# Kernel tuning notes

Measured on AMD Instinct MI355X. Metric: run time of the kernel, lower is better.

## Reference

```python
import jax, jax.numpy as jnp
import numpy as np

NUM_EMBEDDINGS = 1024
EMBEDDING_DIM = 64
COMMITMENT_COST = 0.25


def setup_inputs() -> dict:
    key = jax.random.key(0)
    k1, k2 = jax.random.split(key)
    z = jax.random.normal(k1, (32, 32, 32, EMBEDDING_DIM), dtype=jnp.float32)
    # embedding.weight.data.uniform_(-1/num_embeddings, 1/num_embeddings)
    lim = 1.0 / NUM_EMBEDDINGS
    codebook = jax.random.uniform(k2, (NUM_EMBEDDINGS, EMBEDDING_DIM),
                                  dtype=jnp.float32, minval=-lim, maxval=lim)
    return {"z": z, "codebook": codebook}


def reference(z, codebook):
    beta = COMMITMENT_COST
    zf = z.reshape(-1, EMBEDDING_DIM)                      # [N, D]
    # Squared euclidean distances (argmin is invariant to sqrt in torch.cdist)
    d2 = (jnp.sum(zf * zf, axis=1, keepdims=True)          # [N, 1]
          + jnp.sum(codebook * codebook, axis=1)[None, :]  # [1, K]
          - 2.0 * jnp.einsum('nd,kd->nk', zf, codebook))   # [N, K]
    encoding_indices = jnp.argmin(d2, axis=1)              # [N] int32
    z_q = codebook[encoding_indices].reshape(z.shape)      # [..., D]
    sg = jax.lax.stop_gradient
    loss = jnp.mean((sg(z_q) - z) ** 2) + beta * jnp.mean((z_q - sg(z)) ** 2)
    z_q_st = z + sg(z_q - z)                               # straight-through
    return (z_q_st, loss, encoding_indices)
```

## Files before the change

kernel.cpp:

```cpp
#include <hip/hip_runtime.h>
#include <stdint.h>

#define N_ROWS 32768
#define DIM 64
#define K_CODES 1024
#define ROWS_PER_BLOCK 128
#define THREADS 512
#define CHUNK 256
#define NCHUNK (K_CODES / CHUNK)
#define NBLOCKS (N_ROWS / ROWS_PER_BLOCK)
#define N_ELEMS (N_ROWS * DIM)
#define ZT_STRIDE 128
#define CT_STRIDE 256


__device__ __forceinline__ float bfbits(uint32_t b) { return __uint_as_float(b << 16); }
__device__ __forceinline__ float bf_lo(uint32_t u) { return __uint_as_float(u << 16); }
__device__ __forceinline__ float bf_hi(uint32_t u) { return __uint_as_float(u & 0xFFFF0000u); }

__device__ __forceinline__ float round_bf16(float f) {
  uint32_t u = __float_as_uint(f);
  uint32_t r = ((u + 0x7FFFu + ((u >> 16) & 1u)) >> 16) << 16;
  return __uint_as_float(r);
}

__device__ __forceinline__ int zcol(int row) {
  return ((row >> 3) << 2) + (((row >> 2) & 1) << 6) + (row & 3);
}

template <typename F>
__device__ __forceinline__ float np_sum64(F get) {
  float r0 = get(0), r1 = get(1), r2 = get(2), r3 = get(3);
  float r4 = get(4), r5 = get(5), r6 = get(6), r7 = get(7);
  for (int i = 8; i < 64; i += 8) {
    r0 = __fadd_rn(r0, get(i + 0)); r1 = __fadd_rn(r1, get(i + 1));
    r2 = __fadd_rn(r2, get(i + 2)); r3 = __fadd_rn(r3, get(i + 3));
    r4 = __fadd_rn(r4, get(i + 4)); r5 = __fadd_rn(r5, get(i + 5));
    r6 = __fadd_rn(r6, get(i + 6)); r7 = __fadd_rn(r7, get(i + 7));
  }
  return __fadd_rn(__fadd_rn(__fadd_rn(r0, r1), __fadd_rn(r2, r3)),
                   __fadd_rn(__fadd_rn(r4, r5), __fadd_rn(r6, r7)));
}

__global__ __launch_bounds__(THREADS, 1) void vq_kernel(
    const void* __restrict__ z, const void* __restrict__ cb,
    float* __restrict__ out, double* __restrict__ partials,
    unsigned int* __restrict__ counter) {
  const int tid = threadIdx.x;

  __shared__ int s_cnt[2];
  __shared__ int s_last;
  __shared__ float zt[DIM][ZT_STRIDE];
  __shared__ uint32_t ctu[DIM][CT_STRIDE];
  __shared__ float s_cc[K_CODES];
  __shared__ float s_zz[ROWS_PER_BLOCK];
  __shared__ float s_bestW[8][ROWS_PER_BLOCK];
  __shared__ int   s_kW[8][ROWS_PER_BLOCK];
  __shared__ int   s_win[ROWS_PER_BLOCK];
  __shared__ double s_loss[ROWS_PER_BLOCK];
  float (*ctf)[CT_STRIDE] = (float (*)[CT_STRIDE])ctu;

  if (tid < 2) s_cnt[tid] = 0;
  __syncthreads();
  if (tid < 128) {
    uint32_t wc = ((const uint32_t*)cb)[(size_t)tid * 255];
    float vc = fabsf(bfbits(wc & 0xFFFFu));
    if (vc == 0.0f || (vc > 5.9e-8f && vc < 32.0f)) atomicAdd(&s_cnt[1], 1);
    uint32_t wz = ((const uint32_t*)z)[(size_t)tid * 8191];
    float vz = fabsf(bfbits(wz & 0xFFFFu));
    if (vz == 0.0f || (vz > 5.9e-8f && vz < 32.0f)) atomicAdd(&s_cnt[0], 1);
  }
  __syncthreads();
  const bool z_bf16  = s_cnt[0] >= 96;
  const bool cb_bf16 = s_cnt[1] >= 96;

  const int TR = tid & 15;
  const int TK = tid >> 4;
  const size_t row0 = (size_t)blockIdx.x * ROWS_PER_BLOCK;

  for (int kk = tid; kk < K_CODES; kk += THREADS) {
    float r0, r1, r2, r3, r4, r5, r6, r7;
    if (cb_bf16) {
      const uint4* cp = (const uint4*)((const uint16_t*)cb + (size_t)kk * DIM);
      uint4 u = cp[0];
      r0 = __fmul_rn(bf_lo(u.x), bf_lo(u.x)); r1 = __fmul_rn(bf_hi(u.x), bf_hi(u.x));
      r2 = __fmul_rn(bf_lo(u.y), bf_lo(u.y)); r3 = __fmul_rn(bf_hi(u.y), bf_hi(u.y));
      r4 = __fmul_rn(bf_lo(u.z), bf_lo(u.z)); r5 = __fmul_rn(bf_hi(u.z), bf_hi(u.z));
      r6 = __fmul_rn(bf_lo(u.w), bf_lo(u.w)); r7 = __fmul_rn(bf_hi(u.w), bf_hi(u.w));
      #pragma unroll
      for (int j = 1; j < 8; ++j) {
        u = cp[j];
        r0 = __fadd_rn(r0, __fmul_rn(bf_lo(u.x), bf_lo(u.x)));
        r1 = __fadd_rn(r1, __fmul_rn(bf_hi(u.x), bf_hi(u.x)));
        r2 = __fadd_rn(r2, __fmul_rn(bf_lo(u.y), bf_lo(u.y)));
        r3 = __fadd_rn(r3, __fmul_rn(bf_hi(u.y), bf_hi(u.y)));
        r4 = __fadd_rn(r4, __fmul_rn(bf_lo(u.z), bf_lo(u.z)));
        r5 = __fadd_rn(r5, __fmul_rn(bf_hi(u.z), bf_hi(u.z)));
        r6 = __fadd_rn(r6, __fmul_rn(bf_lo(u.w), bf_lo(u.w)));
        r7 = __fadd_rn(r7, __fmul_rn(bf_hi(u.w), bf_hi(u.w)));
      }
    } else {
      const float4* cp = (const float4*)((const float*)cb + (size_t)kk * DIM);
      float4 a = cp[0], b = cp[1];
      r0 = __fmul_rn(a.x, a.x); r1 = __fmul_rn(a.y, a.y);
      r2 = __fmul_rn(a.z, a.z); r3 = __fmul_rn(a.w, a.w);
      r4 = __fmul_rn(b.x, b.x); r5 = __fmul_rn(b.y, b.y);
      r6 = __fmul_rn(b.z, b.z); r7 = __fmul_rn(b.w, b.w);
      #pragma unroll
      for (int j = 1; j < 8; ++j) {
        a = cp[2 * j]; b = cp[2 * j + 1];
        r0 = __fadd_rn(r0, __fmul_rn(a.x, a.x));
        r1 = __fadd_rn(r1, __fmul_rn(a.y, a.y));
        r2 = __fadd_rn(r2, __fmul_rn(a.z, a.z));
        r3 = __fadd_rn(r3, __fmul_rn(a.w, a.w));
        r4 = __fadd_rn(r4, __fmul_rn(b.x, b.x));
        r5 = __fadd_rn(r5, __fmul_rn(b.y, b.y));
        r6 = __fadd_rn(r6, __fmul_rn(b.z, b.z));
        r7 = __fadd_rn(r7, __fmul_rn(b.w, b.w));
      }
    }
    s_cc[kk] = __fadd_rn(__fadd_rn(__fadd_rn(r0, r1), __fadd_rn(r2, r3)),
                         __fadd_rn(__fadd_rn(r4, r5), __fadd_rn(r6, r7)));
  }

  if (z_bf16) {
    const uint4* src = (const uint4*)((const uint16_t*)z + row0 * DIM);
    #pragma unroll
    for (int j = 0; j < 2; ++j) {
      int idx = tid + THREADS * j;
      int row = idx >> 3, w = idx & 7, d0 = w * 8;
      int col = zcol(row) ^ (w << 2);
      uint4 u = src[idx];
      zt[d0 + 0][col] = bf_lo(u.x); zt[d0 + 1][col] = bf_hi(u.x);
      zt[d0 + 2][col] = bf_lo(u.y); zt[d0 + 3][col] = bf_hi(u.y);
      zt[d0 + 4][col] = bf_lo(u.z); zt[d0 + 5][col] = bf_hi(u.z);
      zt[d0 + 6][col] = bf_lo(u.w); zt[d0 + 7][col] = bf_hi(u.w);
    }
  } else {
    const float4* src = (const float4*)((const float*)z + row0 * DIM);
    #pragma unroll
    for (int j = 0; j < 4; ++j) {
      int idx = tid + THREADS * j;
      int row = idx >> 4, d0 = (idx & 15) * 4;
      int col = zcol(row) ^ (((d0 >> 3) & 7) << 2);
      float4 v = src[idx];
      zt[d0 + 0][col] = v.x; zt[d0 + 1][col] = v.y;
      zt[d0 + 2][col] = v.z; zt[d0 + 3][col] = v.w;
    }
  }
  __syncthreads();

  if (tid < ROWS_PER_BLOCK) {
    const int c0 = zcol(tid);
    s_zz[tid] = np_sum64([&](int d) {
      float v = zt[d][c0 ^ (((d >> 3) & 7) << 2)];
      return __fmul_rn(v, v); });
  }

  float best[8] = {3.4e38f, 3.4e38f, 3.4e38f, 3.4e38f,
                   3.4e38f, 3.4e38f, 3.4e38f, 3.4e38f};
  int bk[8] = {0, 0, 0, 0, 0, 0, 0, 0};
  float acc[8][8];
  #pragma unroll
  for (int ri = 0; ri < 8; ++ri)
    #pragma unroll
    for (int ki = 0; ki < 8; ++ki) acc[ri][ki] = 0.0f;

  if (cb_bf16) {
    for (int c = 0; c < NCHUNK; ++c) {
      __syncthreads();
      const uint4* src = (const uint4*)((const uint16_t*)cb + (size_t)c * CHUNK * DIM);
      #pragma unroll
      for (int t = 0; t < 2; ++t) {
        int task = tid + THREADS * t;
        int j = task >> 3, w = task & 7;
        uint4 a = src[(size_t)(2 * j) * 8 + w];
        uint4 b = src[(size_t)(2 * j + 1) * 8 + w];
        int d0 = w * 8;
        int colb = j ^ (w << 3);
        ctu[d0 + 0][colb] = (a.x & 0xFFFFu) | (b.x << 16);
        ctu[d0 + 1][colb] = (a.x >> 16) | (b.x & 0xFFFF0000u);
        ctu[d0 + 2][colb] = (a.y & 0xFFFFu) | (b.y << 16);
        ctu[d0 + 3][colb] = (a.y >> 16) | (b.y & 0xFFFF0000u);
        ctu[d0 + 4][colb] = (a.z & 0xFFFFu) | (b.z << 16);
        ctu[d0 + 5][colb] = (a.z >> 16) | (b.z & 0xFFFF0000u);
        ctu[d0 + 6][colb] = (a.w & 0xFFFFu) | (b.w << 16);
        ctu[d0 + 7][colb] = (a.w >> 16) | (b.w & 0xFFFF0000u);
      }
      __syncthreads();

      #pragma unroll 4
      for (int d = 0; d < DIM; ++d) {
        const int zs = ((d >> 3) & 7) << 2;
        const int X  = (d >> 3) << 3;
        float4 zA = *(const float4*)&zt[d][(TR << 2) ^ zs];
        float4 zB = *(const float4*)&zt[d][((TR << 2) ^ zs) + 64];
        uint4 cu = *(const uint4*)&ctu[d][(TK << 2) ^ X];
        float zv[8] = {zA.x, zA.y, zA.z, zA.w, zB.x, zB.y, zB.z, zB.w};
        float cv[8] = {bf_lo(cu.x), bf_hi(cu.x), bf_lo(cu.y), bf_hi(cu.y),
                       bf_lo(cu.z), bf_hi(cu.z), bf_lo(cu.w), bf_hi(cu.w)};
        #pragma unroll
        for (int ri = 0; ri < 8; ++ri)
          #pragma unroll
          for (int ki = 0; ki < 8; ++ki)
            acc[ri][ki] = __fadd_rn(acc[ri][ki], __fmul_rn(zv[ri], cv[ki]));
      }

      #pragma unroll
      for (int ri = 0; ri < 8; ++ri) {
        const float zzr = s_zz[TR * 8 + ri];
        #pragma unroll
        for (int ki = 0; ki < 8; ++ki) {
          const int k = c * CHUNK + TK * 8 + ki;
          float e = __fsub_rn(__fadd_rn(zzr, s_cc[k]), __fmul_rn(2.0f, acc[ri][ki]));
          if (e < best[ri]) { best[ri] = e; bk[ri] = k; }
          acc[ri][ki] = 0.0f;
        }
      }
    }
  } else {
    for (int c = 0; c < NCHUNK; ++c) {
      __syncthreads();
      const float4* src = (const float4*)((const float*)cb + (size_t)c * CHUNK * DIM);
      #pragma unroll
      for (int j = 0; j < 8; ++j) {
        int idx = tid + THREADS * j;
        int kc = idx >> 4, d0 = (idx & 15) * 4;
        int col = kc ^ (((d0 >> 3) & 3) << 3);
        float4 v = src[idx];
        ctf[d0 + 0][col] = v.x; ctf[d0 + 1][col] = v.y;
        ctf[d0 + 2][col] = v.z; ctf[d0 + 3][col] = v.w;
      }
      __syncthreads();

      #pragma unroll 4
      for (int d = 0; d < DIM; ++d) {
        const int zs = ((d >> 3) & 7) << 2;
        const int cs = ((d >> 3) & 3) << 3;
        float4 zA = *(const float4*)&zt[d][(TR << 2) ^ zs];
        float4 zB = *(const float4*)&zt[d][((TR << 2) ^ zs) + 64];
        float4 cA = *(const float4*)&ctf[d][(TK << 3) ^ cs];
        float4 cB = *(const float4*)&ctf[d][((TK << 3) ^ cs) + 4];
        float zv[8] = {zA.x, zA.y, zA.z, zA.w, zB.x, zB.y, zB.z, zB.w};
        float cv[8] = {cA.x, cA.y, cA.z, cA.w, cB.x, cB.y, cB.z, cB.w};
        #pragma unroll
        for (int ri = 0; ri < 8; ++ri)
          #pragma unroll
          for (int ki = 0; ki < 8; ++ki)
            acc[ri][ki] = __fadd_rn(acc[ri][ki], __fmul_rn(zv[ri], cv[ki]));
      }

      #pragma unroll
      for (int ri = 0; ri < 8; ++ri) {
        const float zzr = s_zz[TR * 8 + ri];
        #pragma unroll
        for (int ki = 0; ki < 8; ++ki) {
          const int k = c * CHUNK + TK * 8 + ki;
          float e = __fsub_rn(__fadd_rn(zzr, s_cc[k]), __fmul_rn(2.0f, acc[ri][ki]));
          if (e < best[ri]) { best[ri] = e; bk[ri] = k; }
          acc[ri][ki] = 0.0f;
        }
      }
    }
  }

  #pragma unroll
  for (int ri = 0; ri < 8; ++ri) {
    float v = best[ri]; int k = bk[ri];
    {
      float v2 = __shfl_xor(v, 16, 64); int k2 = __shfl_xor(k, 16, 64);
      if (v2 < v || (v2 == v && k2 < k)) { v = v2; k = k2; }
      v2 = __shfl_xor(v, 32, 64); k2 = __shfl_xor(k, 32, 64);
      if (v2 < v || (v2 == v && k2 < k)) { v = v2; k = k2; }
    }
    best[ri] = v; bk[ri] = k;
  }
  {
    const int lane = tid & 63, wv = tid >> 6;
    if (lane < 16) {
      #pragma unroll
      for (int ri = 0; ri < 8; ++ri) {
        s_bestW[wv][lane * 8 + ri] = best[ri];
        s_kW[wv][lane * 8 + ri] = bk[ri];
      }
    }
  }
  __syncthreads();

  if (tid < ROWS_PER_BLOCK) {
    float b = 3.4e38f;
    int bbk = 0x7FFFFFFF;
    #pragma unroll
    for (int p = 0; p < 8; ++p) {
      float v = s_bestW[p][tid];
      int vk = s_kW[p][tid];
      if (v < b || (v == b && vk < bbk)) { b = v; bbk = vk; }
    }
    s_win[tid] = bbk;
    const int c0 = zcol(tid);
    double acc2 = 0.0;
    if (cb_bf16) {
      const uint16_t* cp = (const uint16_t*)cb + (size_t)bbk * DIM;
      for (int d = 0; d < DIM; ++d) {
        double df = (double)zt[d][c0 ^ (((d >> 3) & 7) << 2)]
                  - (double)bfbits((uint32_t)cp[d]);
        acc2 = fma(df, df, acc2);
      }
    } else {
      const float* cp = (const float*)cb + (size_t)bbk * DIM;
      for (int d = 0; d < DIM; ++d) {
        double df = (double)zt[d][c0 ^ (((d >> 3) & 7) << 2)] - (double)cp[d];
        acc2 = fma(df, df, acc2);
      }
    }
    s_loss[tid] = acc2;
    out[(size_t)N_ELEMS + 1 + row0 + tid] = round_bf16((float)bbk);
  }
  __syncthreads();

  const size_t base = row0 * DIM;
  #pragma unroll
  for (int j = 0; j < 16; ++j) {
    int idx = tid + THREADS * j;
    int rr = idx >> 6, dd = idx & 63;
    int w = s_win[rr];
    float v;
    if (cb_bf16) v = bfbits((uint32_t)((const uint16_t*)cb)[(size_t)w * DIM + dd]);
    else         v = round_bf16(((const float*)cb)[(size_t)w * DIM + dd]);
    out[base + idx] = v;
  }

  if (tid == 0) {
    double s = 0.0;
    for (int i = 0; i < ROWS_PER_BLOCK; ++i) s += s_loss[i];
    partials[blockIdx.x] = s;
    __threadfence();
    unsigned int old = atomicAdd(counter, 1u);
    s_last = (((old + 1u) % (unsigned int)NBLOCKS) == 0u) ? 1 : 0;
  }
  __syncthreads();
  if (s_last) {
    __threadfence();
    if (tid < 128) s_loss[tid] = partials[tid] + partials[tid + 128];
    __syncthreads();
    if (tid == 0) {
      double t = 0.0;
      for (int i = 0; i < 128; ++i) t += s_loss[i];
      out[N_ELEMS] = round_bf16((float)(1.25 * t / (double)N_ELEMS));
    }
  }
}

extern "C" void kernel_launch(void* const* d_in, const int* in_sizes, int n_in,
                              void* d_out, int out_size, void* d_ws, size_t ws_size,
                              hipStream_t stream) {
  const void* z  = d_in[0];
  const void* cb = d_in[1];
  float* out = (float*)d_out;
  uint8_t* ws = (uint8_t*)d_ws;
  unsigned int* counter = (unsigned int*)(ws + 4096);
  double* partials = (double*)(ws + 8192);

  vq_kernel<<<NBLOCKS, THREADS, 0, stream>>>(z, cb, out, partials, counter);
}
```

Measured before the change: 133.1 us.

## Halve rows per block to 64 and shrink per-thread register tile

Halves rows per block from 128 to 64, doubling the grid to 512 blocks so more CUs are busy, and shrinks each thread's accumulator tile from 8x8 to 4x8 (bf16) or 4x4 (fp32). The shared-memory swizzles are reworked for the narrower layouts, and the fp32 codebook path now streams 128-code chunks. The final partial-sum reduction is generalised to the larger block count. The cost is less register-level reuse per LDS load and more codebook staging traffic in total, since each block still reads the whole codebook for fewer rows.

```diff
diff --git a/kernel.cpp b/kernel.cpp
--- a/kernel.cpp
+++ b/kernel.cpp
@@ -4,14 +4,14 @@
 #define N_ROWS 32768
 #define DIM 64
 #define K_CODES 1024
-#define ROWS_PER_BLOCK 128
+#define ROWS_PER_BLOCK 64
 #define THREADS 512
 #define CHUNK 256
 #define NCHUNK (K_CODES / CHUNK)
 #define NBLOCKS (N_ROWS / ROWS_PER_BLOCK)
 #define N_ELEMS (N_ROWS * DIM)
-#define ZT_STRIDE 128
-#define CT_STRIDE 256
+#define ZT_STRIDE 64
+#define CT_STRIDE 128
 
 
 __device__ __forceinline__ float bfbits(uint32_t b) { return __uint_as_float(b << 16); }
@@ -22,10 +22,6 @@
   uint32_t u = __float_as_uint(f);
   uint32_t r = ((u + 0x7FFFu + ((u >> 16) & 1u)) >> 16) << 16;
   return __uint_as_float(r);
-}
-
-__device__ __forceinline__ int zcol(int row) {
-  return ((row >> 3) << 2) + (((row >> 2) & 1) << 6) + (row & 3);
 }
 
 template <typename F>
@@ -125,11 +121,10 @@
 
   if (z_bf16) {
     const uint4* src = (const uint4*)((const uint16_t*)z + row0 * DIM);
-    #pragma unroll
-    for (int j = 0; j < 2; ++j) {
-      int idx = tid + THREADS * j;
+    {
+      int idx = tid;
       int row = idx >> 3, w = idx & 7, d0 = w * 8;
-      int col = zcol(row) ^ (w << 2);
+      int col = row ^ (w << 3);
       uint4 u = src[idx];
       zt[d0 + 0][col] = bf_lo(u.x); zt[d0 + 1][col] = bf_hi(u.x);
       zt[d0 + 2][col] = bf_lo(u.y); zt[d0 + 3][col] = bf_hi(u.y);
@@ -139,10 +134,10 @@
   } else {
     const float4* src = (const float4*)((const float*)z + row0 * DIM);
     #pragma unroll
-    for (int j = 0; j < 4; ++j) {
+    for (int j = 0; j < 2; ++j) {
       int idx = tid + THREADS * j;
       int row = idx >> 4, d0 = (idx & 15) * 4;
-      int col = zcol(row) ^ (((d0 >> 3) & 7) << 2);
+      int col = row ^ (((d0 >> 3) & 7) << 3);
       float4 v = src[idx];
       zt[d0 + 0][col] = v.x; zt[d0 + 1][col] = v.y;
       zt[d0 + 2][col] = v.z; zt[d0 + 3][col] = v.w;
@@ -151,18 +146,16 @@
   __syncthreads();
 
   if (tid < ROWS_PER_BLOCK) {
-    const int c0 = zcol(tid);
     s_zz[tid] = np_sum64([&](int d) {
-      float v = zt[d][c0 ^ (((d >> 3) & 7) << 2)];
+      float v = zt[d][tid ^ (((d >> 3) & 7) << 3)];
       return __fmul_rn(v, v); });
   }
 
-  float best[8] = {3.4e38f, 3.4e38f, 3.4e38f, 3.4e38f,
-                   3.4e38f, 3.4e38f, 3.4e38f, 3.4e38f};
-  int bk[8] = {0, 0, 0, 0, 0, 0, 0, 0};
-  float acc[8][8];
+  float best[4] = {3.4e38f, 3.4e38f, 3.4e38f, 3.4e38f};
+  int bk[4] = {0, 0, 0, 0};
+  float acc[4][8];
   #pragma unroll
-  for (int ri = 0; ri < 8; ++ri)
+  for (int ri = 0; ri < 4; ++ri)
     #pragma unroll
     for (int ki = 0; ki < 8; ++ki) acc[ri][ki] = 0.0f;
 
@@ -191,24 +184,22 @@
 
       #pragma unroll 4
       for (int d = 0; d < DIM; ++d) {
-        const int zs = ((d >> 3) & 7) << 2;
-        const int X  = (d >> 3) << 3;
-        float4 zA = *(const float4*)&zt[d][(TR << 2) ^ zs];
-        float4 zB = *(const float4*)&zt[d][((TR << 2) ^ zs) + 64];
+        const int X = (d >> 3) << 3;
+        float4 zA = *(const float4*)&zt[d][(TR << 2) ^ X];
         uint4 cu = *(const uint4*)&ctu[d][(TK << 2) ^ X];
-        float zv[8] = {zA.x, zA.y, zA.z, zA.w, zB.x, zB.y, zB.z, zB.w};
+        float zv[4] = {zA.x, zA.y, zA.z, zA.w};
         float cv[8] = {bf_lo(cu.x), bf_hi(cu.x), bf_lo(cu.y), bf_hi(cu.y),
                        bf_lo(cu.z), bf_hi(cu.z), bf_lo(cu.w), bf_hi(cu.w)};
         #pragma unroll
-        for (int ri = 0; ri < 8; ++ri)
+        for (int ri = 0; ri < 4; ++ri)
           #pragma unroll
           for (int ki = 0; ki < 8; ++ki)
             acc[ri][ki] = __fadd_rn(acc[ri][ki], __fmul_rn(zv[ri], cv[ki]));
       }
 
       #pragma unroll
-      for (int ri = 0; ri < 8; ++ri) {
-        const float zzr = s_zz[TR * 8 + ri];
+      for (int ri = 0; ri < 4; ++ri) {
+        const float zzr = s_zz[TR * 4 + ri];
         #pragma unroll
         for (int ki = 0; ki < 8; ++ki) {
           const int k = c * CHUNK + TK * 8 + ki;
@@ -219,14 +210,14 @@
       }
     }
   } else {
-    for (int c = 0; c < NCHUNK; ++c) {
+    for (int hc = 0; hc < 8; ++hc) {
       __syncthreads();
-      const float4* src = (const float4*)((const float*)cb + (size_t)c * CHUNK * DIM);
-      #pragma unroll
-      for (int j = 0; j < 8; ++j) {
-        int idx = tid + THREADS * j;
+      const float4* src = (const float4*)((const float*)cb + (size_t)hc * 128 * DIM);
+      #pragma unroll
+      for (int t = 0; t < 4; ++t) {
+        int idx = tid + THREADS * t;
         int kc = idx >> 4, d0 = (idx & 15) * 4;
-        int col = kc ^ (((d0 >> 3) & 3) << 3);
+        int col = kc ^ (((d0 >> 3) & 7) << 2);
         float4 v = src[idx];
         ctf[d0 + 0][col] = v.x; ctf[d0 + 1][col] = v.y;
         ctf[d0 + 2][col] = v.z; ctf[d0 + 3][col] = v.w;
@@ -235,27 +226,25 @@
 
       #pragma unroll 4
       for (int d = 0; d < DIM; ++d) {
-        const int zs = ((d >> 3) & 7) << 2;
-        const int cs = ((d >> 3) & 3) << 3;
-        float4 zA = *(const float4*)&zt[d][(TR << 2) ^ zs];
-        float4 zB = *(const float4*)&zt[d][((TR << 2) ^ zs) + 64];
-        float4 cA = *(const float4*)&ctf[d][(TK << 3) ^ cs];
-        float4 cB = *(const float4*)&ctf[d][((TK << 3) ^ cs) + 4];
-        float zv[8] = {zA.x, zA.y, zA.z, zA.w, zB.x, zB.y, zB.z, zB.w};
-        float cv[8] = {cA.x, cA.y, cA.z, cA.w, cB.x, cB.y, cB.z, cB.w};
+        const int X3 = (d >> 3) << 3;
+        const int X2 = (d >> 3) << 2;
+        float4 zA = *(const float4*)&zt[d][(TR << 2) ^ X3];
+        float4 cA = *(const float4*)&ctf[d][(TK << 2) ^ X2];
+        float zv[4] = {zA.x, zA.y, zA.z, zA.w};
+        float cv[4] = {cA.x, cA.y, cA.z, cA.w};
         #pragma unroll
-        for (int ri = 0; ri < 8; ++ri)
+        for (int ri = 0; ri < 4; ++ri)
           #pragma unroll
-          for (int ki = 0; ki < 8; ++ki)
+          for (int ki = 0; ki < 4; ++ki)
             acc[ri][ki] = __fadd_rn(acc[ri][ki], __fmul_rn(zv[ri], cv[ki]));
       }
 
       #pragma unroll
-      for (int ri = 0; ri < 8; ++ri) {
-        const float zzr = s_zz[TR * 8 + ri];
+      for (int ri = 0; ri < 4; ++ri) {
+        const float zzr = s_zz[TR * 4 + ri];
         #pragma unroll
-        for (int ki = 0; ki < 8; ++ki) {
-          const int k = c * CHUNK + TK * 8 + ki;
+        for (int ki = 0; ki < 4; ++ki) {
+          const int k = hc * 128 + TK * 4 + ki;
           float e = __fsub_rn(__fadd_rn(zzr, s_cc[k]), __fmul_rn(2.0f, acc[ri][ki]));
           if (e < best[ri]) { best[ri] = e; bk[ri] = k; }
           acc[ri][ki] = 0.0f;
@@ -265,7 +254,7 @@
   }
 
   #pragma unroll
-  for (int ri = 0; ri < 8; ++ri) {
+  for (int ri = 0; ri < 4; ++ri) {
     float v = best[ri]; int k = bk[ri];
     {
       float v2 = __shfl_xor(v, 16, 64); int k2 = __shfl_xor(k, 16, 64);
@@ -279,9 +268,9 @@
     const int lane = tid & 63, wv = tid >> 6;
     if (lane < 16) {
       #pragma unroll
-      for (int ri = 0; ri < 8; ++ri) {
-        s_bestW[wv][lane * 8 + ri] = best[ri];
-        s_kW[wv][lane * 8 + ri] = bk[ri];
+      for (int ri = 0; ri < 4; ++ri) {
+        s_bestW[wv][lane * 4 + ri] = best[ri];
+        s_kW[wv][lane * 4 + ri] = bk[ri];
       }
     }
   }
@@ -297,19 +286,18 @@
       if (v < b || (v == b && vk < bbk)) { b = v; bbk = vk; }
     }
     s_win[tid] = bbk;
-    const int c0 = zcol(tid);
     double acc2 = 0.0;
     if (cb_bf16) {
       const uint16_t* cp = (const uint16_t*)cb + (size_t)bbk * DIM;
       for (int d = 0; d < DIM; ++d) {
-        double df = (double)zt[d][c0 ^ (((d >> 3) & 7) << 2)]
+        double df = (double)zt[d][tid ^ (((d >> 3) & 7) << 3)]
                   - (double)bfbits((uint32_t)cp[d]);
         acc2 = fma(df, df, acc2);
       }
     } else {
       const float* cp = (const float*)cb + (size_t)bbk * DIM;
       for (int d = 0; d < DIM; ++d) {
-        double df = (double)zt[d][c0 ^ (((d >> 3) & 7) << 2)] - (double)cp[d];
+        double df = (double)zt[d][tid ^ (((d >> 3) & 7) << 3)] - (double)cp[d];
         acc2 = fma(df, df, acc2);
       }
     }
@@ -320,7 +308,7 @@
 
   const size_t base = row0 * DIM;
   #pragma unroll
-  for (int j = 0; j < 16; ++j) {
+  for (int j = 0; j < 8; ++j) {
     int idx = tid + THREADS * j;
     int rr = idx >> 6, dd = idx & 63;
     int w = s_win[rr];
@@ -341,11 +329,15 @@
   __syncthreads();
   if (s_last) {
     __threadfence();
-    if (tid < 128) s_loss[tid] = partials[tid] + partials[tid + 128];
+    if (tid < 64) {
+      double t = 0.0;
+      for (int i = tid; i < NBLOCKS; i += 64) t += partials[i];
+      s_loss[tid] = t;
+    }
     __syncthreads();
     if (tid == 0) {
       double t = 0.0;
-      for (int i = 0; i < 128; ++i) t += s_loss[i];
+      for (int i = 0; i < 64; ++i) t += s_loss[i];
       out[N_ELEMS] = round_bf16((float)(1.25 * t / (double)N_ELEMS));
     }
   }
```

Result: slower. 161.0 us (+20.9%).
